# Kernel optimization log

Hardware: AMD Instinct MI355X
Metric: run time of the kernel (lower is better)

The kernel has to match this reference:

```python
import jax, jax.numpy as jnp
import numpy as np

N = 100000
E = 500000
F_IN = 128
HID = 64
HEADS = 4
OUT = 32
NEG_SLOPE = 0.2


def _glorot(key, shape):
    fan_in, fan_out = shape[0], shape[1]
    lim = jnp.sqrt(6.0 / (fan_in + fan_out))
    return jax.random.uniform(key, shape, jnp.float32, -lim, lim)


def setup_inputs() -> dict:
    key = jax.random.key(0)
    ks = jax.random.split(key, 20)
    x = jax.random.normal(ks[0], (N, F_IN), jnp.float32)
    edge_index = jax.random.randint(ks[1], (2, E), 0, N, jnp.int64)
    edge_attr = jax.random.uniform(ks[2], (E, 1), jnp.float32)
    d1 = HEADS * HID
    params = {
        # conv1: F_IN -> HEADS x HID
        "Wl1": _glorot(ks[3], (F_IN, d1)), "bl1": jnp.zeros((d1,), jnp.float32),
        "Wr1": _glorot(ks[4], (F_IN, d1)), "br1": jnp.zeros((d1,), jnp.float32),
        "We1": _glorot(ks[5], (1, d1)),
        "att1": _glorot(ks[6], (HEADS, HID)),
        "b1": jnp.zeros((d1,), jnp.float32),
        "Wl2": _glorot(ks[7], (d1, OUT)), "bl2": jnp.zeros((OUT,), jnp.float32),
        "Wr2": _glorot(ks[8], (d1, OUT)), "br2": jnp.zeros((OUT,), jnp.float32),
        "We2": _glorot(ks[9], (1, OUT)),
        "att2": _glorot(ks[10], (1, OUT)),
        "b2": jnp.zeros((OUT,), jnp.float32),
    }
    return {"x": x, "edge_index": edge_index, "edge_attr": edge_attr, **params}


def gatv2_conv(x, src, dst, edge_attr, Wl, bl, Wr, br, We, att, bias, heads, out_ch):
    """PyG GATv2Conv (add_self_loops=False, concat=True, share_weights=False)."""
    n = x.shape[0]
    xl = (x @ Wl + bl).reshape(n, heads, out_ch)          # source transform
    xr = (x @ Wr + br).reshape(n, heads, out_ch)          # target transform
    e = (edge_attr @ We).reshape(-1, heads, out_ch)       # [E, H, C]
    m = jax.nn.leaky_relu(xl[src] + xr[dst] + e, NEG_SLOPE)  # [E, H, C]
    alpha = jnp.einsum('ehc,hc->eh', m, att)              # [E, H]
    # softmax over edges sharing the same destination node
    amax = jax.ops.segment_max(alpha, dst, num_segments=n)
    ealpha = jnp.exp(alpha - amax[dst])
    denom = jax.ops.segment_sum(ealpha, dst, num_segments=n)
    alpha = ealpha / (denom[dst] + 1e-16)
    out = jax.ops.segment_sum(xl[src] * alpha[:, :, None], dst, num_segments=n)
    return out.reshape(n, heads * out_ch) + bias


def reference(x, edge_index, edge_attr, Wl1, bl1, Wr1, br1, We1, att1, b1,
              Wl2, bl2, Wr2, br2, We2, att2, b2):
    src, dst = edge_index[0], edge_index[1]
    h = gatv2_conv(x, src, dst, edge_attr, Wl1, bl1, Wr1, br1, We1, att1, b1, HEADS, HID)
    h = jax.nn.relu(h)  # dropout is identity at inference
    out = gatv2_conv(h, src, dst, edge_attr, Wl2, bl2, Wr2, br2, We2, att2, b2, 1, OUT)
    return out
```

## Files before the change

### kernel.cpp

```cpp
#include <hip/hip_runtime.h>
#include <cstddef>
#include <cstdint>

#define F_IN 128
#define D1   256
#define HEADS 4
#define HID   64
#define OUT_C 32
#define NEG   0.2f

typedef unsigned short ushort_t;
typedef __attribute__((ext_vector_type(8))) short short8;
typedef __attribute__((ext_vector_type(4))) float f32x4;
typedef __attribute__((ext_vector_type(4))) unsigned short ushort4v;
typedef __attribute__((ext_vector_type(8))) unsigned short ushort8v;

__device__ __forceinline__ float bu2f(ushort_t u) {
  return __uint_as_float(((unsigned)u) << 16);
}
__device__ __forceinline__ ushort_t f2bu(float f) {
  unsigned u = __float_as_uint(f);
  return (ushort_t)((u + 0x7FFF + ((u >> 16) & 1)) >> 16);
}

__global__ void prep_b1_k(const float* __restrict__ Wl, const float* __restrict__ Wr,
                          const float* __restrict__ bl, const float* __restrict__ br,
                          ushort_t* __restrict__ Bt, float* __restrict__ biasc) {
  int i = blockIdx.x * blockDim.x + threadIdx.x;
  int nn = i >> 7, k = i & 127;
  float v = (nn < D1) ? Wl[(size_t)k * D1 + nn] : Wr[(size_t)k * D1 + (nn - D1)];
  Bt[(size_t)nn * F_IN + k] = f2bu(v);
  if (k == 0) biasc[nn] = (nn < D1) ? bl[nn] : br[nn - D1];
}

__global__ void prep_b2_k(const float* __restrict__ Wl, const float* __restrict__ Wr,
                          const float* __restrict__ bl, const float* __restrict__ br,
                          ushort_t* __restrict__ Bt, float* __restrict__ biasc) {
  int i = blockIdx.x * blockDim.x + threadIdx.x;
  int nn = i >> 8, k = i & 255;
  float v = (nn < OUT_C) ? Wl[(size_t)k * OUT_C + nn] : Wr[(size_t)k * OUT_C + (nn - OUT_C)];
  Bt[(size_t)nn * D1 + k] = f2bu(v);
  if (k == 0) biasc[nn] = (nn < OUT_C) ? bl[nn] : br[nn - OUT_C];
}

__global__ void gemm1_fused(const float* __restrict__ A, const ushort_t* __restrict__ Bt,
                            const float* __restrict__ biasc, ushort_t* __restrict__ C,
                            int M) {
  __shared__ ushort_t As[128][136];
  __shared__ ushort_t Bs[64][136];
  const int tid = threadIdx.x;
  const int wave = tid >> 6, lane = tid & 63;
  const int wm = wave & 1, wn = wave >> 1;
  const int quad = lane >> 4, l16 = lane & 15;
  const int m0 = blockIdx.x * 128;
  for (int i = tid; i < 128 * 16; i += 256) {
    int r = i >> 4, ch = i & 15;
    int gr = m0 + r;
    f32x4 v0 = {}, v1 = {};
    if (gr < M) {
      const float* p = A + (size_t)gr * 128 + ch * 8;
      v0 = *(const f32x4*)p;
      v1 = *(const f32x4*)(p + 4);
    }
    short8 o;
    o[0] = (short)f2bu(v0[0]); o[1] = (short)f2bu(v0[1]);
    o[2] = (short)f2bu(v0[2]); o[3] = (short)f2bu(v0[3]);
    o[4] = (short)f2bu(v1[0]); o[5] = (short)f2bu(v1[1]);
    o[6] = (short)f2bu(v1[2]); o[7] = (short)f2bu(v1[3]);
    *(short8*)(&As[r][ch * 8]) = o;
  }
  __syncthreads();
  for (int nt = 0; nt < 8; ++nt) {
    for (int i = tid; i < 64 * 16; i += 256) {
      int r = i >> 4, ch = i & 15;
      *(short8*)(&Bs[r][ch * 8]) =
          *(const short8*)(Bt + ((nt * 64 + r) << 7) + ch * 8);
    }
    __syncthreads();
    f32x4 acc[4][2] = {};
#pragma unroll
    for (int ks = 0; ks < 128; ks += 32) {
      short8 af[4], bfr[2];
#pragma unroll
      for (int mi = 0; mi < 4; ++mi)
        af[mi] = *(const short8*)(&As[wm * 64 + mi * 16 + l16][ks + quad * 8]);
#pragma unroll
      for (int ni = 0; ni < 2; ++ni)
        bfr[ni] = *(const short8*)(&Bs[wn * 32 + ni * 16 + l16][ks + quad * 8]);
#pragma unroll
      for (int mi = 0; mi < 4; ++mi)
#pragma unroll
        for (int ni = 0; ni < 2; ++ni)
          acc[mi][ni] = __builtin_amdgcn_mfma_f32_16x16x32_bf16(af[mi], bfr[ni],
                                                                acc[mi][ni], 0, 0, 0);
    }
#pragma unroll
    for (int mi = 0; mi < 4; ++mi) {
#pragma unroll
      for (int r = 0; r < 4; ++r) {
        int grow = m0 + wm * 64 + mi * 16 + quad * 4 + r;
        if (grow >= M) continue;
#pragma unroll
        for (int ni = 0; ni < 2; ++ni) {
          int gcol = nt * 64 + wn * 32 + ni * 16 + l16;
          C[(size_t)grow * 512 + gcol] = f2bu(acc[mi][ni][r] + biasc[gcol]);
        }
      }
    }
    __syncthreads();
  }
}

template <int WM, int WN, int BK>
__global__ void mfma_gemm(const ushort_t* __restrict__ A16, const ushort_t* __restrict__ Bt,
                          const float* __restrict__ biasc, ushort_t* __restrict__ C,
                          int M, int N, int K) {
  constexpr int BM = WM * 64, BN = WN * 64;
  constexpr int LD = BK + 8;
  constexpr int CPR = BK / 8;
  __shared__ ushort_t As[BM][LD];
  __shared__ ushort_t Bs[BN][LD];
  const int tid = threadIdx.x;
  const int wave = tid >> 6, lane = tid & 63;
  const int wm = wave % WM, wn = wave / WM;
  const int quad = lane >> 4, l16 = lane & 15;
  const int m0 = blockIdx.x * BM, n0 = blockIdx.y * BN;
  const int nth = WM * WN * 64;
  f32x4 acc[4][4] = {};
  for (int k0 = 0; k0 < K; k0 += BK) {
    for (int i = tid; i < BM * CPR; i += nth) {
      int r = i / CPR, ch = i % CPR;
      int gr = m0 + r;
      short8 v = {};
      if (gr < M) v = *(const short8*)(A16 + (size_t)gr * K + k0 + ch * 8);
      *(short8*)(&As[r][ch * 8]) = v;
    }
    for (int i = tid; i < BN * CPR; i += nth) {
      int r = i / CPR, ch = i % CPR;
      short8 v = {};
      if (n0 + r < N) v = *(const short8*)(Bt + (size_t)(n0 + r) * K + k0 + ch * 8);
      *(short8*)(&Bs[r][ch * 8]) = v;
    }
    __syncthreads();
#pragma unroll
    for (int ks = 0; ks < BK; ks += 32) {
      short8 af[4], bfr[4];
#pragma unroll
      for (int mi = 0; mi < 4; ++mi)
        af[mi] = *(const short8*)(&As[wm * 64 + mi * 16 + l16][ks + quad * 8]);
#pragma unroll
      for (int ni = 0; ni < 4; ++ni)
        bfr[ni] = *(const short8*)(&Bs[wn * 64 + ni * 16 + l16][ks + quad * 8]);
#pragma unroll
      for (int mi = 0; mi < 4; ++mi)
#pragma unroll
        for (int ni = 0; ni < 4; ++ni)
          acc[mi][ni] = __builtin_amdgcn_mfma_f32_16x16x32_bf16(af[mi], bfr[ni],
                                                                acc[mi][ni], 0, 0, 0);
    }
    __syncthreads();
  }
#pragma unroll
  for (int mi = 0; mi < 4; ++mi) {
#pragma unroll
    for (int r = 0; r < 4; ++r) {
      int grow = m0 + wm * 64 + mi * 16 + quad * 4 + r;
      if (grow >= M) continue;
#pragma unroll
      for (int ni = 0; ni < 4; ++ni) {
        int gcol = n0 + wn * 64 + ni * 16 + l16;
        if (gcol < N) C[(size_t)grow * N + gcol] = f2bu(acc[mi][ni][r] + biasc[gcol]);
      }
    }
  }
}

__global__ void hist_k(const int* __restrict__ dst, int* __restrict__ deg, int e) {
  int i = blockIdx.x * blockDim.x + threadIdx.x;
  if (i < e) atomicAdd(&deg[dst[i]], 1);
}

__global__ void scan_block_k(const int* __restrict__ deg, int* __restrict__ row_ptr,
                             int* __restrict__ bsum, int n) {
  __shared__ int s[1024];
  int i = blockIdx.x * 1024 + threadIdx.x;
  int v = (i < n) ? deg[i] : 0;
  s[threadIdx.x] = v;
  __syncthreads();
  for (int off = 1; off < 1024; off <<= 1) {
    int t = (threadIdx.x >= off) ? s[threadIdx.x - off] : 0;
    __syncthreads();
    s[threadIdx.x] += t;
    __syncthreads();
  }
  if (i < n) row_ptr[i + 1] = s[threadIdx.x];
  if (threadIdx.x == 1023) bsum[blockIdx.x] = s[1023];
}

__global__ void scan_bsum_k(int* __restrict__ bsum, int nb) {
  __shared__ int s[128];
  int v = (threadIdx.x < nb) ? bsum[threadIdx.x] : 0;
  s[threadIdx.x] = v;
  __syncthreads();
  for (int off = 1; off < 128; off <<= 1) {
    int t = (threadIdx.x >= off) ? s[threadIdx.x - off] : 0;
    __syncthreads();
    s[threadIdx.x] += t;
    __syncthreads();
  }
  if (threadIdx.x < nb) bsum[threadIdx.x] = s[threadIdx.x] - v;
}

__global__ void add_off_k(int* __restrict__ row_ptr, const int* __restrict__ bsum,
                          int* __restrict__ cursor, int n) {
  int i = blockIdx.x * blockDim.x + threadIdx.x;
  if (i == 0) { row_ptr[0] = 0; cursor[0] = 0; }
  if (i < n) {
    int v = row_ptr[i + 1] + bsum[i >> 10];
    row_ptr[i + 1] = v;
    if (i + 1 < n) cursor[i + 1] = v;
  }
}

__global__ void fill_k(const int* __restrict__ src, const int* __restrict__ dst,
                       const float* __restrict__ eattr, int* __restrict__ cursor,
                       int2* __restrict__ csr, int e) {
  int i = blockIdx.x * blockDim.x + threadIdx.x;
  if (i >= e) return;
  int p = atomicAdd(&cursor[dst[i]], 1);
  csr[p] = make_int2(src[i], __float_as_int(eattr[i]));
}

__global__ void gat1_k(const int* __restrict__ row_ptr, const int2* __restrict__ csr,
                       const ushort_t* __restrict__ C1,
                       const float* __restrict__ We, const float* __restrict__ att,
                       const float* __restrict__ bias, ushort_t* __restrict__ h1, int n) {
  int lane = threadIdx.x & 63;
  int node = (int)((((size_t)blockIdx.x * blockDim.x + threadIdx.x)) >> 5);
  if (node >= n) return;
  int cb = (lane & 31) * 8;
  ushort8v xr8 = *(const ushort8v*)(C1 + (node << 9) + 256 + cb);
  f32x4 w0 = *(const f32x4*)(We + cb),  w1 = *(const f32x4*)(We + cb + 4);
  f32x4 a0 = *(const f32x4*)(att + cb), a1 = *(const f32x4*)(att + cb + 4);
  float xrr[8], Wev[8], attv[8], acc[8];
  float esum = 0.f;
#pragma unroll
  for (int j = 0; j < 4; ++j) {
    Wev[j] = w0[j]; Wev[j + 4] = w1[j];
    attv[j] = a0[j]; attv[j + 4] = a1[j];
  }
#pragma unroll
  for (int j = 0; j < 8; ++j) { xrr[j] = bu2f(xr8[j]); acc[j] = 0.f; }
  int p = row_ptr[node], p1 = row_ptr[node + 1];
  for (; p + 2 <= p1; p += 2) {
    int2 e0 = csr[p], e1 = csr[p + 1];
    ushort8v g0 = *(const ushort8v*)(C1 + (e0.x << 9) + cb);
    ushort8v g1 = *(const ushort8v*)(C1 + (e1.x << 9) + cb);
    float wg0 = __int_as_float(e0.y), wg1 = __int_as_float(e1.y);
    float xv0[8], xv1[8], v0 = 0.f, v1 = 0.f;
#pragma unroll
    for (int j = 0; j < 8; ++j) {
      xv0[j] = bu2f(g0[j]);
      float m = xv0[j] + xrr[j] + wg0 * Wev[j];
      m = m > 0.f ? m : NEG * m;
      v0 += m * attv[j];
      xv1[j] = bu2f(g1[j]);
      float q = xv1[j] + xrr[j] + wg1 * Wev[j];
      q = q > 0.f ? q : NEG * q;
      v1 += q * attv[j];
    }
    v0 += __shfl_xor(v0, 1, 64); v1 += __shfl_xor(v1, 1, 64);
    v0 += __shfl_xor(v0, 2, 64); v1 += __shfl_xor(v1, 2, 64);
    v0 += __shfl_xor(v0, 4, 64); v1 += __shfl_xor(v1, 4, 64);
    float eh0 = __expf(v0), eh1 = __expf(v1);
    esum += eh0 + eh1;
#pragma unroll
    for (int j = 0; j < 8; ++j) acc[j] += eh0 * xv0[j] + eh1 * xv1[j];
  }
  if (p < p1) {
    int2 e0 = csr[p];
    ushort8v g0 = *(const ushort8v*)(C1 + (e0.x << 9) + cb);
    float wg0 = __int_as_float(e0.y);
    float xv0[8], v0 = 0.f;
#pragma unroll
    for (int j = 0; j < 8; ++j) {
      xv0[j] = bu2f(g0[j]);
      float m = xv0[j] + xrr[j] + wg0 * Wev[j];
      m = m > 0.f ? m : NEG * m;
      v0 += m * attv[j];
    }
    v0 += __shfl_xor(v0, 1, 64);
    v0 += __shfl_xor(v0, 2, 64);
    v0 += __shfl_xor(v0, 4, 64);
    float eh0 = __expf(v0);
    esum += eh0;
#pragma unroll
    for (int j = 0; j < 8; ++j) acc[j] += eh0 * xv0[j];
  }
  f32x4 b0 = *(const f32x4*)(bias + cb), b1 = *(const f32x4*)(bias + cb + 4);
  float inv = 1.f / (esum + 1e-16f);
  ushort8v o;
#pragma unroll
  for (int j = 0; j < 8; ++j) {
    float bb = j < 4 ? b0[j] : b1[j - 4];
    float t = acc[j] * inv + bb;
    o[j] = f2bu(t > 0.f ? t : 0.f);
  }
  *(ushort8v*)(h1 + (node << 8) + cb) = o;
}

__global__ void gat2_k(const int* __restrict__ row_ptr, const int2* __restrict__ csr,
                       const ushort_t* __restrict__ C2,
                       const float* __restrict__ We, const float* __restrict__ att,
                       const float* __restrict__ bias, float* __restrict__ out, int n) {
  size_t t = (size_t)blockIdx.x * blockDim.x + threadIdx.x;
  int node = (int)(t >> 3);
  int g = (int)(t & 7);
  if (node >= n) return;
  int cb = g * 4;
  ushort4v xr4 = *(const ushort4v*)(C2 + (node << 6) + 32 + cb);
  f32x4 wv = *(const f32x4*)(We + cb);
  f32x4 av = *(const f32x4*)(att + cb);
  float xrr[4], acc[4] = {0.f, 0.f, 0.f, 0.f};
  float esum = 0.f;
#pragma unroll
  for (int j = 0; j < 4; ++j) xrr[j] = bu2f(xr4[j]);
  int p = row_ptr[node], p1 = row_ptr[node + 1];
  for (; p + 4 <= p1; p += 4) {
    int2 ee[4];
#pragma unroll
    for (int u = 0; u < 4; ++u) ee[u] = csr[p + u];
    ushort4v xl4[4];
#pragma unroll
    for (int u = 0; u < 4; ++u)
      xl4[u] = *(const ushort4v*)(C2 + (ee[u].x << 6) + cb);
    float xv[4][4], v[4];
#pragma unroll
    for (int u = 0; u < 4; ++u) {
      float wgt = __int_as_float(ee[u].y);
      v[u] = 0.f;
#pragma unroll
      for (int j = 0; j < 4; ++j) {
        xv[u][j] = bu2f(xl4[u][j]);
        float m = xv[u][j] + xrr[j] + wgt * wv[j];
        m = m > 0.f ? m : NEG * m;
        v[u] += m * av[j];
      }
    }
#pragma unroll
    for (int u = 0; u < 4; ++u) {
      v[u] += __shfl_xor(v[u], 1, 64);
      v[u] += __shfl_xor(v[u], 2, 64);
      v[u] += __shfl_xor(v[u], 4, 64);
    }
#pragma unroll
    for (int u = 0; u < 4; ++u) {
      float eh = __expf(v[u]);
      esum += eh;
#pragma unroll
      for (int j = 0; j < 4; ++j) acc[j] += eh * xv[u][j];
    }
  }
  for (; p < p1; ++p) {
    int2 ed = csr[p];
    float wgt = __int_as_float(ed.y);
    ushort4v xl4 = *(const ushort4v*)(C2 + (ed.x << 6) + cb);
    float xv[4], v = 0.f;
#pragma unroll
    for (int j = 0; j < 4; ++j) {
      xv[j] = bu2f(xl4[j]);
      float m = xv[j] + xrr[j] + wgt * wv[j];
      m = m > 0.f ? m : NEG * m;
      v += m * av[j];
    }
    v += __shfl_xor(v, 1, 64);
    v += __shfl_xor(v, 2, 64);
    v += __shfl_xor(v, 4, 64);
    float eh = __expf(v);
    esum += eh;
#pragma unroll
    for (int j = 0; j < 4; ++j) acc[j] += eh * xv[j];
  }
  f32x4 bv = *(const f32x4*)(bias + cb);
  float inv = 1.f / (esum + 1e-16f);
  f32x4 ov;
#pragma unroll
  for (int j = 0; j < 4; ++j) ov[j] = acc[j] * inv + bv[j];
  *(f32x4*)(out + (size_t)node * OUT_C + cb) = ov;
}

extern "C" void kernel_launch(void* const* d_in, const int* in_sizes, int n_in,
                              void* d_out, int out_size, void* d_ws, size_t ws_size,
                              hipStream_t stream) {
  const float* x     = (const float*)d_in[0];
  const int*   eidx  = (const int*)d_in[1];
  const float* eattr = (const float*)d_in[2];
  const float* Wl1 = (const float*)d_in[3];
  const float* bl1 = (const float*)d_in[4];
  const float* Wr1 = (const float*)d_in[5];
  const float* br1 = (const float*)d_in[6];
  const float* We1 = (const float*)d_in[7];
  const float* att1 = (const float*)d_in[8];
  const float* b1  = (const float*)d_in[9];
  const float* Wl2 = (const float*)d_in[10];
  const float* bl2 = (const float*)d_in[11];
  const float* Wr2 = (const float*)d_in[12];
  const float* br2 = (const float*)d_in[13];
  const float* We2 = (const float*)d_in[14];
  const float* att2 = (const float*)d_in[15];
  const float* b2  = (const float*)d_in[16];

  const int n = in_sizes[0] / F_IN;
  const int e = in_sizes[2];
  const int* src = eidx;
  const int* dst = eidx + e;
  float* out = (float*)d_out;

  char* w = (char*)d_ws;
  ushort_t* C1   = (ushort_t*)w;  w += (size_t)n * 512 * 2;
  ushort_t* h1b  = (ushort_t*)w;  w += (size_t)n * D1 * 2;
  ushort_t* C2   = (ushort_t*)w;  w += (size_t)n * 64 * 2;
  ushort_t* Bt1  = (ushort_t*)w;  w += 512 * F_IN * 2;
  ushort_t* Bt2  = (ushort_t*)w;  w += 64 * D1 * 2;
  float* bias1c  = (float*)w;     w += 512 * 4;
  float* bias2c  = (float*)w;     w += 64 * 4;
  int2*  csr     = (int2*)w;      w += (size_t)e * 8;
  int*   row_ptr = (int*)w;       w += ((size_t)n + 1) * 4;
  int*   cursor  = (int*)w;       w += (size_t)n * 4;
  int*   bsum    = (int*)w;       w += 512;
  int*   deg = cursor;

  dim3 blk(256);
  const int nb = (n + 1023) / 1024;

  prep_b1_k<<<(512 * 128) / 256, blk, 0, stream>>>(Wl1, Wr1, bl1, br1, Bt1, bias1c);
  prep_b2_k<<<(64 * 256) / 256, blk, 0, stream>>>(Wl2, Wr2, bl2, br2, Bt2, bias2c);

  hipMemsetAsync(deg, 0, (size_t)n * sizeof(int), stream);
  hist_k<<<(e + 255) / 256, blk, 0, stream>>>(dst, deg, e);
  scan_block_k<<<nb, 1024, 0, stream>>>(deg, row_ptr, bsum, n);
  scan_bsum_k<<<1, 128, 0, stream>>>(bsum, nb);
  add_off_k<<<(n + 255) / 256, blk, 0, stream>>>(row_ptr, bsum, cursor, n);
  fill_k<<<(e + 255) / 256, blk, 0, stream>>>(src, dst, eattr, cursor, csr, e);

  gemm1_fused<<<(n + 127) / 128, blk, 0, stream>>>(x, Bt1, bias1c, C1, n);
  gat1_k<<<((size_t)n * 32 + 255) / 256, blk, 0, stream>>>(row_ptr, csr, C1,
                                                           We1, att1, b1, h1b, n);

  mfma_gemm<2, 1, 64><<<dim3((n + 127) / 128, 1), dim3(128), 0, stream>>>(
      h1b, Bt2, bias2c, C2, n, 64, D1);
  gat2_k<<<((size_t)n * 8 + 255) / 256, blk, 0, stream>>>(row_ptr, csr, C2,
                                                          We2, att2, b2, out, n);
}
```

Measured before the change: 388.6 us.

## Merge prep and scan kernels, replace fused gemm1 with templated 2D-grid GEMM

Merges the two weight-prep kernels into one launch and replaces the three-kernel prefix scan with a single-block serial-chunk scan, cutting launch count. The first-layer GEMM now uses the generic MFMA GEMM with an fp32-to-bf16 conversion path and a 2D grid over 4 column tiles, instead of one block looping over 8 column tiles. This trades re-reading x across column blocks for more parallelism. The single-block scan walks about 98 chunks sequentially, which may be slower than the multi-block version.

Result: slower. 554.1 us (+42.6%).

```diff
diff --git a/kernel.cpp b/kernel.cpp
--- a/kernel.cpp
+++ b/kernel.cpp
@@ -23,96 +23,29 @@
   return (ushort_t)((u + 0x7FFF + ((u >> 16) & 1)) >> 16);
 }
 
-__global__ void prep_b1_k(const float* __restrict__ Wl, const float* __restrict__ Wr,
-                          const float* __restrict__ bl, const float* __restrict__ br,
-                          ushort_t* __restrict__ Bt, float* __restrict__ biasc) {
+__global__ void prep_k(const float* __restrict__ Wl1, const float* __restrict__ Wr1,
+                       const float* __restrict__ bl1, const float* __restrict__ br1,
+                       const float* __restrict__ Wl2, const float* __restrict__ Wr2,
+                       const float* __restrict__ bl2, const float* __restrict__ br2,
+                       ushort_t* __restrict__ Bt1, float* __restrict__ bias1,
+                       ushort_t* __restrict__ Bt2, float* __restrict__ bias2) {
   int i = blockIdx.x * blockDim.x + threadIdx.x;
-  int nn = i >> 7, k = i & 127;
-  float v = (nn < D1) ? Wl[(size_t)k * D1 + nn] : Wr[(size_t)k * D1 + (nn - D1)];
-  Bt[(size_t)nn * F_IN + k] = f2bu(v);
-  if (k == 0) biasc[nn] = (nn < D1) ? bl[nn] : br[nn - D1];
-}
-
-__global__ void prep_b2_k(const float* __restrict__ Wl, const float* __restrict__ Wr,
-                          const float* __restrict__ bl, const float* __restrict__ br,
-                          ushort_t* __restrict__ Bt, float* __restrict__ biasc) {
-  int i = blockIdx.x * blockDim.x + threadIdx.x;
-  int nn = i >> 8, k = i & 255;
-  float v = (nn < OUT_C) ? Wl[(size_t)k * OUT_C + nn] : Wr[(size_t)k * OUT_C + (nn - OUT_C)];
-  Bt[(size_t)nn * D1 + k] = f2bu(v);
-  if (k == 0) biasc[nn] = (nn < OUT_C) ? bl[nn] : br[nn - OUT_C];
-}
-
-__global__ void gemm1_fused(const float* __restrict__ A, const ushort_t* __restrict__ Bt,
-                            const float* __restrict__ biasc, ushort_t* __restrict__ C,
-                            int M) {
-  __shared__ ushort_t As[128][136];
-  __shared__ ushort_t Bs[64][136];
-  const int tid = threadIdx.x;
-  const int wave = tid >> 6, lane = tid & 63;
-  const int wm = wave & 1, wn = wave >> 1;
-  const int quad = lane >> 4, l16 = lane & 15;
-  const int m0 = blockIdx.x * 128;
-  for (int i = tid; i < 128 * 16; i += 256) {
-    int r = i >> 4, ch = i & 15;
-    int gr = m0 + r;
-    f32x4 v0 = {}, v1 = {};
-    if (gr < M) {
-      const float* p = A + (size_t)gr * 128 + ch * 8;
-      v0 = *(const f32x4*)p;
-      v1 = *(const f32x4*)(p + 4);
-    }
-    short8 o;
-    o[0] = (short)f2bu(v0[0]); o[1] = (short)f2bu(v0[1]);
-    o[2] = (short)f2bu(v0[2]); o[3] = (short)f2bu(v0[3]);
-    o[4] = (short)f2bu(v1[0]); o[5] = (short)f2bu(v1[1]);
-    o[6] = (short)f2bu(v1[2]); o[7] = (short)f2bu(v1[3]);
-    *(short8*)(&As[r][ch * 8]) = o;
-  }
-  __syncthreads();
-  for (int nt = 0; nt < 8; ++nt) {
-    for (int i = tid; i < 64 * 16; i += 256) {
-      int r = i >> 4, ch = i & 15;
-      *(short8*)(&Bs[r][ch * 8]) =
-          *(const short8*)(Bt + ((nt * 64 + r) << 7) + ch * 8);
-    }
-    __syncthreads();
-    f32x4 acc[4][2] = {};
-#pragma unroll
-    for (int ks = 0; ks < 128; ks += 32) {
-      short8 af[4], bfr[2];
-#pragma unroll
-      for (int mi = 0; mi < 4; ++mi)
-        af[mi] = *(const short8*)(&As[wm * 64 + mi * 16 + l16][ks + quad * 8]);
-#pragma unroll
-      for (int ni = 0; ni < 2; ++ni)
-        bfr[ni] = *(const short8*)(&Bs[wn * 32 + ni * 16 + l16][ks + quad * 8]);
-#pragma unroll
-      for (int mi = 0; mi < 4; ++mi)
-#pragma unroll
-        for (int ni = 0; ni < 2; ++ni)
-          acc[mi][ni] = __builtin_amdgcn_mfma_f32_16x16x32_bf16(af[mi], bfr[ni],
-                                                                acc[mi][ni], 0, 0, 0);
-    }
-#pragma unroll
-    for (int mi = 0; mi < 4; ++mi) {
-#pragma unroll
-      for (int r = 0; r < 4; ++r) {
-        int grow = m0 + wm * 64 + mi * 16 + quad * 4 + r;
-        if (grow >= M) continue;
-#pragma unroll
-        for (int ni = 0; ni < 2; ++ni) {
-          int gcol = nt * 64 + wn * 32 + ni * 16 + l16;
-          C[(size_t)grow * 512 + gcol] = f2bu(acc[mi][ni][r] + biasc[gcol]);
-        }
-      }
-    }
-    __syncthreads();
-  }
-}
-
-template <int WM, int WN, int BK>
-__global__ void mfma_gemm(const ushort_t* __restrict__ A16, const ushort_t* __restrict__ Bt,
+  if (i < 512 * 128) {
+    int nn = i >> 7, k = i & 127;
+    float v = (nn < D1) ? Wl1[(size_t)k * D1 + nn] : Wr1[(size_t)k * D1 + (nn - D1)];
+    Bt1[(size_t)nn * F_IN + k] = f2bu(v);
+    if (k == 0) bias1[nn] = (nn < D1) ? bl1[nn] : br1[nn - D1];
+  } else {
+    int j = i - 512 * 128;
+    int nn = j >> 8, k = j & 255;
+    float v = (nn < OUT_C) ? Wl2[(size_t)k * OUT_C + nn] : Wr2[(size_t)k * OUT_C + (nn - OUT_C)];
+    Bt2[(size_t)nn * D1 + k] = f2bu(v);
+    if (k == 0) bias2[nn] = (nn < OUT_C) ? bl2[nn] : br2[nn - OUT_C];
+  }
+}
+
+template <int WM, int WN, int BK, bool CVT>
+__global__ void mfma_gemm(const void* __restrict__ Av, const ushort_t* __restrict__ Bt,
                           const float* __restrict__ biasc, ushort_t* __restrict__ C,
                           int M, int N, int K) {
   constexpr int BM = WM * 64, BN = WN * 64;
@@ -131,9 +64,26 @@
     for (int i = tid; i < BM * CPR; i += nth) {
       int r = i / CPR, ch = i % CPR;
       int gr = m0 + r;
-      short8 v = {};
-      if (gr < M) v = *(const short8*)(A16 + (size_t)gr * K + k0 + ch * 8);
-      *(short8*)(&As[r][ch * 8]) = v;
+      if (CVT) {
+        const float* A32 = (const float*)Av;
+        f32x4 v0 = {}, v1 = {};
+        if (gr < M) {
+          const float* p = A32 + (size_t)gr * K + k0 + ch * 8;
+          v0 = *(const f32x4*)p;
+          v1 = *(const f32x4*)(p + 4);
+        }
+        short8 o;
+        o[0] = (short)f2bu(v0[0]); o[1] = (short)f2bu(v0[1]);
+        o[2] = (short)f2bu(v0[2]); o[3] = (short)f2bu(v0[3]);
+        o[4] = (short)f2bu(v1[0]); o[5] = (short)f2bu(v1[1]);
+        o[6] = (short)f2bu(v1[2]); o[7] = (short)f2bu(v1[3]);
+        *(short8*)(&As[r][ch * 8]) = o;
+      } else {
+        const ushort_t* A16 = (const ushort_t*)Av;
+        short8 v = {};
+        if (gr < M) v = *(const short8*)(A16 + (size_t)gr * K + k0 + ch * 8);
+        *(short8*)(&As[r][ch * 8]) = v;
+      }
     }
     for (int i = tid; i < BN * CPR; i += nth) {
       int r = i / CPR, ch = i % CPR;
@@ -180,45 +130,31 @@
   if (i < e) atomicAdd(&deg[dst[i]], 1);
 }
 
-__global__ void scan_block_k(const int* __restrict__ deg, int* __restrict__ row_ptr,
-                             int* __restrict__ bsum, int n) {
+__global__ void scan_all_k(const int* __restrict__ deg, int* __restrict__ row_ptr,
+                           int* __restrict__ cursor, int n, int nb) {
   __shared__ int s[1024];
-  int i = blockIdx.x * 1024 + threadIdx.x;
-  int v = (i < n) ? deg[i] : 0;
-  s[threadIdx.x] = v;
+  __shared__ int carry;
+  if (threadIdx.x == 0) { carry = 0; row_ptr[0] = 0; cursor[0] = 0; }
   __syncthreads();
-  for (int off = 1; off < 1024; off <<= 1) {
-    int t = (threadIdx.x >= off) ? s[threadIdx.x - off] : 0;
-    __syncthreads();
-    s[threadIdx.x] += t;
-    __syncthreads();
-  }
-  if (i < n) row_ptr[i + 1] = s[threadIdx.x];
-  if (threadIdx.x == 1023) bsum[blockIdx.x] = s[1023];
-}
-
-__global__ void scan_bsum_k(int* __restrict__ bsum, int nb) {
-  __shared__ int s[128];
-  int v = (threadIdx.x < nb) ? bsum[threadIdx.x] : 0;
-  s[threadIdx.x] = v;
-  __syncthreads();
-  for (int off = 1; off < 128; off <<= 1) {
-    int t = (threadIdx.x >= off) ? s[threadIdx.x - off] : 0;
-    __syncthreads();
-    s[threadIdx.x] += t;
-    __syncthreads();
-  }
-  if (threadIdx.x < nb) bsum[threadIdx.x] = s[threadIdx.x] - v;
-}
-
-__global__ void add_off_k(int* __restrict__ row_ptr, const int* __restrict__ bsum,
-                          int* __restrict__ cursor, int n) {
-  int i = blockIdx.x * blockDim.x + threadIdx.x;
-  if (i == 0) { row_ptr[0] = 0; cursor[0] = 0; }
-  if (i < n) {
-    int v = row_ptr[i + 1] + bsum[i >> 10];
-    row_ptr[i + 1] = v;
-    if (i + 1 < n) cursor[i + 1] = v;
+  for (int c = 0; c < nb; ++c) {
+    int i = c * 1024 + threadIdx.x;
+    int v = (i < n) ? deg[i] : 0;
+    s[threadIdx.x] = v;
+    __syncthreads();
+    for (int off = 1; off < 1024; off <<= 1) {
+      int t = (threadIdx.x >= off) ? s[threadIdx.x - off] : 0;
+      __syncthreads();
+      s[threadIdx.x] += t;
+      __syncthreads();
+    }
+    int incl = s[threadIdx.x] + carry;
+    if (i < n) {
+      row_ptr[i + 1] = incl;
+      if (i + 1 < n) cursor[i + 1] = incl;
+    }
+    __syncthreads();
+    if (threadIdx.x == 1023) carry = incl;
+    __syncthreads();
   }
 }
 
@@ -427,27 +363,25 @@
   int2*  csr     = (int2*)w;      w += (size_t)e * 8;
   int*   row_ptr = (int*)w;       w += ((size_t)n + 1) * 4;
   int*   cursor  = (int*)w;       w += (size_t)n * 4;
-  int*   bsum    = (int*)w;       w += 512;
-  int*   deg = cursor;
+  int*   deg     = (int*)w;       w += (size_t)n * 4;
 
   dim3 blk(256);
   const int nb = (n + 1023) / 1024;
 
-  prep_b1_k<<<(512 * 128) / 256, blk, 0, stream>>>(Wl1, Wr1, bl1, br1, Bt1, bias1c);
-  prep_b2_k<<<(64 * 256) / 256, blk, 0, stream>>>(Wl2, Wr2, bl2, br2, Bt2, bias2c);
+  prep_k<<<(512 * 128 + 64 * 256 + 255) / 256, blk, 0, stream>>>(
+      Wl1, Wr1, bl1, br1, Wl2, Wr2, bl2, br2, Bt1, bias1c, Bt2, bias2c);
 
   hipMemsetAsync(deg, 0, (size_t)n * sizeof(int), stream);
   hist_k<<<(e + 255) / 256, blk, 0, stream>>>(dst, deg, e);
-  scan_block_k<<<nb, 1024, 0, stream>>>(deg, row_ptr, bsum, n);
-  scan_bsum_k<<<1, 128, 0, stream>>>(bsum, nb);
-  add_off_k<<<(n + 255) / 256, blk, 0, stream>>>(row_ptr, bsum, cursor, n);
+  scan_all_k<<<1, 1024, 0, stream>>>(deg, row_ptr, cursor, n, nb);
   fill_k<<<(e + 255) / 256, blk, 0, stream>>>(src, dst, eattr, cursor, csr, e);
 
-  gemm1_fused<<<(n + 127) / 128, blk, 0, stream>>>(x, Bt1, bias1c, C1, n);
+  mfma_gemm<2, 2, 64, true><<<dim3((n + 127) / 128, 4), blk, 0, stream>>>(
+      x, Bt1, bias1c, C1, n, 512, F_IN);
   gat1_k<<<((size_t)n * 32 + 255) / 256, blk, 0, stream>>>(row_ptr, csr, C1,
                                                            We1, att1, b1, h1b, n);
 
-  mfma_gemm<2, 1, 64><<<dim3((n + 127) / 128, 1), dim3(128), 0, stream>>>(
+  mfma_gemm<2, 1, 64, false><<<dim3((n + 127) / 128, 1), dim3(128), 0, stream>>>(
       h1b, Bt2, bias2c, C2, n, 64, D1);
   gat2_k<<<((size_t)n * 8 + 255) / 256, blk, 0, stream>>>(row_ptr, csr, C2,
                                                           We2, att2, b2, out, n);
```
